# Kernel tuning notes

Measured on AMD Instinct MI355X. Metric: run time of the kernel, lower is better.

The kernel has to match this reference:

```python
import jax, jax.numpy as jnp
import numpy as np

U, I, D = 100000, 100000, 64
B, T = 16384, 1_638_400
R = 5  # rating levels 1..5


def setup_inputs() -> dict:
    key = jax.random.key(0)
    ks = jax.random.split(key, 8)
    return {
        "user_idx": jax.random.randint(ks[0], (B,), 0, U, dtype=jnp.int32),
        "item_idx": jax.random.randint(ks[1], (B,), 0, I, dtype=jnp.int32),
        "flat_items": jax.random.randint(ks[2], (T,), 0, I, dtype=jnp.int32),
        "seg_ids": jnp.sort(jax.random.randint(ks[3], (T,), 0, B * R, dtype=jnp.int32)),
        "user_emb": (jax.random.uniform(ks[4], (U, D), dtype=jnp.float32) - 0.5) * 0.01,
        "item_emb": (jax.random.uniform(ks[5], (I, D), dtype=jnp.float32) - 0.5) * 0.01,
        "Mr": (jax.random.uniform(ks[6], (I, D), dtype=jnp.float32) - 0.5) * 0.01,
        "user_bias": jnp.zeros((U,), dtype=jnp.float32),
        "item_bias": jnp.zeros((I,), dtype=jnp.float32),
        "global_avg": jnp.float32(3.5),
    }


def reference(user_idx, item_idx, flat_items, seg_ids, user_emb, item_emb, Mr, user_bias, item_bias, global_avg):
    num_seg = B * R  # segment = sample_i * 5 + (rating - 1)
    # Original torch code does Mr_ik(rate_dict).sum() -> scalar over ALL dims,
    # then broadcasts that scalar onto the latent_dim vector UuMpc[i].
    row_sum = Mr[flat_items].sum(axis=-1)  # [T] per-item full-row sum
    # Emulate `rate_dict.remove(item_idx[i])`: mask out the target item of this sample.
    match = flat_items == item_idx[seg_ids // R]  # [T]
    contrib = jnp.where(match, 0.0, row_sum)
    seg_sum = jax.ops.segment_sum(contrib, seg_ids, num_segments=num_seg)  # [B*5]
    cnt = jax.ops.segment_sum(jnp.where(match, 0.0, 1.0), seg_ids, num_segments=num_seg)
    per_seg = jnp.where(cnt > 0, seg_sum / jnp.sqrt(jnp.maximum(cnt, 1.0)), 0.0)
    uu_mpc = per_seg.reshape(B, R).sum(axis=-1)  # [B] scalar per sample
    user_vec = user_emb[user_idx] + uu_mpc[:, None]  # broadcast scalar over latent dim
    item_vec = item_emb[item_idx]
    rui = (user_vec * item_vec).sum(axis=-1) + user_bias[user_idx] + item_bias[item_idx] + global_avg
    return jnp.clip(rui, 1.0, 5.0)
```

## Files before the change

kernel.cpp:

```cpp
#include <hip/hip_runtime.h>

#define U_N 100000
#define I_N 100000
#define D_N 64
#define B_N 16384
#define T_N 1638400
#define R_N 5

#define RS_THREADS (I_N * 16)
#define BD_THREADS (T_N / 4)
#define K1_THREADS (RS_THREADS + BD_THREADS)

__global__ void prep_kernel(const float* __restrict__ Mr,
                            const int* __restrict__ seg_ids,
                            float* __restrict__ rowsum,
                            int* __restrict__ sample_start) {
    int gtid = blockIdx.x * blockDim.x + threadIdx.x;
    if (gtid < RS_THREADS) {
        int row = gtid >> 4;
        int sub = gtid & 15;
        const float4* p = (const float4*)(Mr + (long)row * D_N);
        float4 v4 = p[sub];
        float v = v4.x + v4.y + v4.z + v4.w;
        v += __shfl_xor(v, 1);
        v += __shfl_xor(v, 2);
        v += __shfl_xor(v, 4);
        v += __shfl_xor(v, 8);
        if (sub == 0) rowsum[row] = v;
    } else {
        int t4 = gtid - RS_THREADS;
        if (t4 >= BD_THREADS) return;
        int base = t4 * 4;
        int4 s4 = ((const int4*)seg_ids)[t4];
        int sv[5];
        sv[0] = (base == 0) ? -1 : seg_ids[base - 1];
        sv[1] = s4.x; sv[2] = s4.y; sv[3] = s4.z; sv[4] = s4.w;
        #pragma unroll
        for (int j = 0; j < 4; ++j) {
            int sp = sv[j], sc = sv[j + 1];
            if (sc > sp) {
                int b_lo = (sp + 5) / 5;
                int b_hi = sc / 5;
                for (int b = b_lo; b <= b_hi; ++b) sample_start[b] = base + j;
            }
        }
        if (base + 4 == T_N) {
            for (int b = sv[4] / 5 + 1; b <= B_N; ++b) sample_start[b] = T_N;
        }
    }
}

__global__ void sample_kernel(const int* __restrict__ user_idx,
                              const int* __restrict__ item_idx,
                              const int* __restrict__ flat_items,
                              const int* __restrict__ seg_ids,
                              const float* __restrict__ user_emb,
                              const float* __restrict__ item_emb,
                              const float* __restrict__ user_bias,
                              const float* __restrict__ item_bias,
                              const float* __restrict__ global_avg,
                              const float* __restrict__ rowsum,
                              const int* __restrict__ sample_start,
                              float* __restrict__ out) {
    __shared__ float s_sum[4][5];
    __shared__ int   s_cnt[4][5];

    int w    = threadIdx.x >> 6;
    int lane = threadIdx.x & 63;
    int b    = blockIdx.x * 4 + w;
    if (b >= B_N) return;

    if (lane < R_N) { s_sum[w][lane] = 0.f; s_cnt[w][lane] = 0; }
    __syncthreads();

    int lo = sample_start[b];
    int hi = sample_start[b + 1];
    int target = item_idx[b];

    for (int t = lo + lane; t < hi; t += 64) {
        int sg = seg_ids[t];
        int it = flat_items[t];
        if (it != target) {
            int r = sg - b * R_N;
            atomicAdd(&s_sum[w][r], rowsum[it]);
            atomicAdd(&s_cnt[w][r], 1);
        }
    }
    __syncthreads();

    float uu = 0.f;
    if (lane == 0) {
        #pragma unroll
        for (int r = 0; r < R_N; ++r) {
            int c = s_cnt[w][r];
            if (c > 0) uu += s_sum[w][r] / sqrtf((float)c);
        }
    }

    int u = user_idx[b];
    float ue = user_emb[(long)u * D_N + lane];
    float ie = item_emb[(long)target * D_N + lane];
    float dot = ue * ie;
    float isum = ie;
    #pragma unroll
    for (int off = 32; off >= 1; off >>= 1) {
        dot  += __shfl_xor(dot, off);
        isum += __shfl_xor(isum, off);
    }
    if (lane == 0) {
        float rui = dot + uu * isum + user_bias[u] + item_bias[target] + global_avg[0];
        rui = fminf(fmaxf(rui, 1.0f), 5.0f);
        out[b] = rui;
    }
}

extern "C" void kernel_launch(void* const* d_in, const int* in_sizes, int n_in,
                              void* d_out, int out_size, void* d_ws, size_t ws_size,
                              hipStream_t stream) {
    const int*   user_idx   = (const int*)d_in[0];
    const int*   item_idx   = (const int*)d_in[1];
    const int*   flat_items = (const int*)d_in[2];
    const int*   seg_ids    = (const int*)d_in[3];
    const float* user_emb   = (const float*)d_in[4];
    const float* item_emb   = (const float*)d_in[5];
    const float* Mr         = (const float*)d_in[6];
    const float* user_bias  = (const float*)d_in[7];
    const float* item_bias  = (const float*)d_in[8];
    const float* global_avg = (const float*)d_in[9];
    float* out = (float*)d_out;

    float* rowsum       = (float*)d_ws;
    int*   sample_start = (int*)(rowsum + I_N);

    prep_kernel<<<(K1_THREADS + 255) / 256, 256, 0, stream>>>(
        Mr, seg_ids, rowsum, sample_start);
    sample_kernel<<<B_N / 4, 256, 0, stream>>>(
        user_idx, item_idx, flat_items, seg_ids, user_emb, item_emb,
        user_bias, item_bias, global_avg, rowsum, sample_start, out);
}
```

Before: 147.3 us.

## Replace shared-memory atomics with register accumulators and wave shuffle reductions

Per-rating sums and counts are now kept in per-lane registers and reduced across the wavefront with shuffles, replacing the LDS atomics and both block-wide barriers. The segment loop is unrolled four ways so several seg_ids, flat_items and rowsum gathers are in flight at once, and the embedding loads are hoisted ahead of the loop to overlap their latency. In exchange, the final reduction now runs ten extra shuffle chains and each lane uses more registers.

```diff
diff --git a/kernel.cpp b/kernel.cpp
--- a/kernel.cpp
+++ b/kernel.cpp
@@ -62,52 +62,67 @@
                               const float* __restrict__ rowsum,
                               const int* __restrict__ sample_start,
                               float* __restrict__ out) {
-    __shared__ float s_sum[4][5];
-    __shared__ int   s_cnt[4][5];
-
-    int w    = threadIdx.x >> 6;
     int lane = threadIdx.x & 63;
-    int b    = blockIdx.x * 4 + w;
+    int b    = (blockIdx.x * blockDim.x + threadIdx.x) >> 6;
     if (b >= B_N) return;
 
-    if (lane < R_N) { s_sum[w][lane] = 0.f; s_cnt[w][lane] = 0; }
-    __syncthreads();
+    int u      = user_idx[b];
+    int target = item_idx[b];
+    float ue = user_emb[(long)u * D_N + lane];
+    float ie = item_emb[(long)target * D_N + lane];
 
     int lo = sample_start[b];
     int hi = sample_start[b + 1];
-    int target = item_idx[b];
+    int base5 = b * R_N;
 
-    for (int t = lo + lane; t < hi; t += 64) {
-        int sg = seg_ids[t];
-        int it = flat_items[t];
-        if (it != target) {
-            int r = sg - b * R_N;
-            atomicAdd(&s_sum[w][r], rowsum[it]);
-            atomicAdd(&s_cnt[w][r], 1);
+    float acc[R_N] = {0.f, 0.f, 0.f, 0.f, 0.f};
+    float cnt[R_N] = {0.f, 0.f, 0.f, 0.f, 0.f};
+
+    for (int t0 = lo + lane; t0 < hi; t0 += 256) {
+        int  sg[4], fi[4];
+        bool ok[4];
+        #pragma unroll
+        for (int k = 0; k < 4; ++k) {
+            int t = t0 + 64 * k;
+            ok[k] = (t < hi);
+            if (ok[k]) { sg[k] = seg_ids[t]; fi[k] = flat_items[t]; }
         }
-    }
-    __syncthreads();
-
-    float uu = 0.f;
-    if (lane == 0) {
+        float rv[4];
         #pragma unroll
-        for (int r = 0; r < R_N; ++r) {
-            int c = s_cnt[w][r];
-            if (c > 0) uu += s_sum[w][r] / sqrtf((float)c);
+        for (int k = 0; k < 4; ++k) {
+            if (ok[k]) rv[k] = rowsum[fi[k]];
+        }
+        #pragma unroll
+        for (int k = 0; k < 4; ++k) {
+            if (ok[k] && fi[k] != target) {
+                int r = sg[k] - base5;
+                #pragma unroll
+                for (int rr = 0; rr < R_N; ++rr) {
+                    if (r == rr) { acc[rr] += rv[k]; cnt[rr] += 1.f; }
+                }
+            }
         }
     }
 
-    int u = user_idx[b];
-    float ue = user_emb[(long)u * D_N + lane];
-    float ie = item_emb[(long)target * D_N + lane];
     float dot = ue * ie;
     float isum = ie;
     #pragma unroll
     for (int off = 32; off >= 1; off >>= 1) {
+        #pragma unroll
+        for (int rr = 0; rr < R_N; ++rr) {
+            acc[rr] += __shfl_xor(acc[rr], off);
+            cnt[rr] += __shfl_xor(cnt[rr], off);
+        }
         dot  += __shfl_xor(dot, off);
         isum += __shfl_xor(isum, off);
     }
+
     if (lane == 0) {
+        float uu = 0.f;
+        #pragma unroll
+        for (int rr = 0; rr < R_N; ++rr) {
+            if (cnt[rr] > 0.f) uu += acc[rr] / sqrtf(cnt[rr]);
+        }
         float rui = dot + uu * isum + user_bias[u] + item_bias[target] + global_avg[0];
         rui = fminf(fmaxf(rui, 1.0f), 5.0f);
         out[b] = rui;
```

After: 141.1 us. -4.2%, faster.

## Use per-segment offsets and ballot match counting instead of shared atomics

Applied to the files above, without the earlier changes.

The prep kernel now builds per-segment start offsets rather than per-sample offsets. The sample kernel derives each segment's count from those offsets minus a ballot/popcount tally of target-item matches. It then accumulates rowsum times a precomputed rsqrt weight in registers and reduces with shuffles, which removes the seg_ids reads, the LDS atomics and the __syncthreads. The cost is a second pass over flat_items whenever a sample has more than 128 entries, plus extra per-element branching to pick the segment weight.

```diff
diff --git a/kernel.cpp b/kernel.cpp
--- a/kernel.cpp
+++ b/kernel.cpp
@@ -6,6 +6,7 @@
 #define B_N 16384
 #define T_N 1638400
 #define R_N 5
+#define NSEG (B_N * R_N)
 
 #define RS_THREADS (I_N * 16)
 #define BD_THREADS (T_N / 4)
@@ -14,7 +15,7 @@
 __global__ void prep_kernel(const float* __restrict__ Mr,
                             const int* __restrict__ seg_ids,
                             float* __restrict__ rowsum,
-                            int* __restrict__ sample_start) {
+                            int* __restrict__ seg_start) {
     int gtid = blockIdx.x * blockDim.x + threadIdx.x;
     if (gtid < RS_THREADS) {
         int row = gtid >> 4;
@@ -32,20 +33,32 @@
         if (t4 >= BD_THREADS) return;
         int base = t4 * 4;
         int4 s4 = ((const int4*)seg_ids)[t4];
-        int sv[5];
-        sv[0] = (base == 0) ? -1 : seg_ids[base - 1];
-        sv[1] = s4.x; sv[2] = s4.y; sv[3] = s4.z; sv[4] = s4.w;
+        int sv0 = (base == 0) ? -1 : seg_ids[base - 1];
+        int sv1 = s4.x, sv2 = s4.y, sv3 = s4.z, sv4 = s4.w;
+        for (int s = sv0 + 1; s <= sv1; ++s) seg_start[s] = base + 0;
+        for (int s = sv1 + 1; s <= sv2; ++s) seg_start[s] = base + 1;
+        for (int s = sv2 + 1; s <= sv3; ++s) seg_start[s] = base + 2;
+        for (int s = sv3 + 1; s <= sv4; ++s) seg_start[s] = base + 3;
+        if (base + 4 == T_N) {
+            for (int s = sv4 + 1; s <= NSEG; ++s) seg_start[s] = T_N;
+        }
+    }
+}
+
+__device__ __forceinline__ void count_matches(unsigned long long m, int tb,
+                                              int e0, int e1, int e2, int e3,
+                                              int e4, int e5, int* mcnt) {
+    if (m) {
+        int ea[6] = {e0, e1, e2, e3, e4, e5};
         #pragma unroll
-        for (int j = 0; j < 4; ++j) {
-            int sp = sv[j], sc = sv[j + 1];
-            if (sc > sp) {
-                int b_lo = (sp + 5) / 5;
-                int b_hi = sc / 5;
-                for (int b = b_lo; b <= b_hi; ++b) sample_start[b] = base + j;
+        for (int r = 0; r < 5; ++r) {
+            int a = ea[r] - tb;     a = a < 0 ? 0 : (a > 64 ? 64 : a);
+            int bb = ea[r + 1] - tb; bb = bb < 0 ? 0 : (bb > 64 ? 64 : bb);
+            if (bb > a) {
+                unsigned long long hiM = (bb == 64) ? ~0ULL : ((1ULL << bb) - 1ULL);
+                unsigned long long loM = (1ULL << a) - 1ULL;
+                mcnt[r] += __popcll(m & hiM & ~loM);
             }
-        }
-        if (base + 4 == T_N) {
-            for (int b = sv[4] / 5 + 1; b <= B_N; ++b) sample_start[b] = T_N;
         }
     }
 }
@@ -53,62 +66,95 @@
 __global__ void sample_kernel(const int* __restrict__ user_idx,
                               const int* __restrict__ item_idx,
                               const int* __restrict__ flat_items,
-                              const int* __restrict__ seg_ids,
                               const float* __restrict__ user_emb,
                               const float* __restrict__ item_emb,
                               const float* __restrict__ user_bias,
                               const float* __restrict__ item_bias,
                               const float* __restrict__ global_avg,
                               const float* __restrict__ rowsum,
-                              const int* __restrict__ sample_start,
+                              const int* __restrict__ seg_start,
                               float* __restrict__ out) {
-    __shared__ float s_sum[4][5];
-    __shared__ int   s_cnt[4][5];
-
-    int w    = threadIdx.x >> 6;
     int lane = threadIdx.x & 63;
-    int b    = blockIdx.x * 4 + w;
+    int b    = (blockIdx.x * blockDim.x + threadIdx.x) >> 6;
     if (b >= B_N) return;
 
-    if (lane < R_N) { s_sum[w][lane] = 0.f; s_cnt[w][lane] = 0; }
-    __syncthreads();
+    int u      = user_idx[b];
+    int target = item_idx[b];
+    float ue = user_emb[(long)u * D_N + lane];
+    float ie = item_emb[(long)target * D_N + lane];
 
-    int lo = sample_start[b];
-    int hi = sample_start[b + 1];
-    int target = item_idx[b];
+    int e0 = seg_start[b * R_N + 0];
+    int e1 = seg_start[b * R_N + 1];
+    int e2 = seg_start[b * R_N + 2];
+    int e3 = seg_start[b * R_N + 3];
+    int e4 = seg_start[b * R_N + 4];
+    int e5 = seg_start[b * R_N + 5];
+    int lo = e0, hi = e5;
 
-    for (int t = lo + lane; t < hi; t += 64) {
-        int sg = seg_ids[t];
-        int it = flat_items[t];
-        if (it != target) {
-            int r = sg - b * R_N;
-            atomicAdd(&s_sum[w][r], rowsum[it]);
-            atomicAdd(&s_cnt[w][r], 1);
-        }
+    int t0 = lo + lane, t1 = lo + 64 + lane;
+    bool ok0 = t0 < hi, ok1 = t1 < hi;
+    int fi0 = -1, fi1 = -1;
+    float rv0 = 0.f, rv1 = 0.f;
+    if (ok0) fi0 = flat_items[t0];
+    if (ok1) fi1 = flat_items[t1];
+    if (ok0) rv0 = rowsum[fi0];
+    if (ok1) rv1 = rowsum[fi1];
+
+    int mcnt[5] = {0, 0, 0, 0, 0};
+    unsigned long long m0 = __ballot(ok0 && fi0 == target);
+    unsigned long long m1 = __ballot(ok1 && fi1 == target);
+    count_matches(m0, lo,      e0, e1, e2, e3, e4, e5, mcnt);
+    count_matches(m1, lo + 64, e0, e1, e2, e3, e4, e5, mcnt);
+    for (int tb = lo + 128; tb < hi; tb += 64) {
+        int t = tb + lane;
+        bool ok = t < hi;
+        int fi = ok ? flat_items[t] : -1;
+        unsigned long long m = __ballot(ok && fi == target);
+        count_matches(m, tb, e0, e1, e2, e3, e4, e5, mcnt);
     }
-    __syncthreads();
 
-    float uu = 0.f;
-    if (lane == 0) {
-        #pragma unroll
-        for (int r = 0; r < R_N; ++r) {
-            int c = s_cnt[w][r];
-            if (c > 0) uu += s_sum[w][r] / sqrtf((float)c);
+    int c0 = (e1 - e0) - mcnt[0];
+    int c1 = (e2 - e1) - mcnt[1];
+    int c2 = (e3 - e2) - mcnt[2];
+    int c3 = (e4 - e3) - mcnt[3];
+    int c4 = (e5 - e4) - mcnt[4];
+    float w0 = c0 > 0 ? rsqrtf((float)c0) : 0.f;
+    float w1 = c1 > 0 ? rsqrtf((float)c1) : 0.f;
+    float w2 = c2 > 0 ? rsqrtf((float)c2) : 0.f;
+    float w3 = c3 > 0 ? rsqrtf((float)c3) : 0.f;
+    float w4 = c4 > 0 ? rsqrtf((float)c4) : 0.f;
+
+    float acc = 0.f;
+    if (ok0 && fi0 != target) {
+        float w = t0 >= e1 ? (t0 >= e2 ? (t0 >= e3 ? (t0 >= e4 ? w4 : w3) : w2) : w1) : w0;
+        acc += rv0 * w;
+    }
+    if (ok1 && fi1 != target) {
+        float w = t1 >= e1 ? (t1 >= e2 ? (t1 >= e3 ? (t1 >= e4 ? w4 : w3) : w2) : w1) : w0;
+        acc += rv1 * w;
+    }
+    for (int tb = lo + 128; tb < hi; tb += 64) {
+        int t = tb + lane;
+        if (t < hi) {
+            int fi = flat_items[t];
+            if (fi != target) {
+                float rv = rowsum[fi];
+                float w = t >= e1 ? (t >= e2 ? (t >= e3 ? (t >= e4 ? w4 : w3) : w2) : w1) : w0;
+                acc += rv * w;
+            }
         }
     }
 
-    int u = user_idx[b];
-    float ue = user_emb[(long)u * D_N + lane];
-    float ie = item_emb[(long)target * D_N + lane];
     float dot = ue * ie;
     float isum = ie;
     #pragma unroll
     for (int off = 32; off >= 1; off >>= 1) {
+        acc  += __shfl_xor(acc, off);
         dot  += __shfl_xor(dot, off);
         isum += __shfl_xor(isum, off);
     }
     if (lane == 0) {
-        float rui = dot + uu * isum + user_bias[u] + item_bias[target] + global_avg[0];
+        float rui = dot + acc * isum + user_bias[u] + item_bias[target] + global_avg[0];
         rui = fminf(fmaxf(rui, 1.0f), 5.0f);
         out[b] = rui;
     }
@@ -129,12 +175,12 @@
     const float* global_avg = (const float*)d_in[9];
     float* out = (float*)d_out;
 
-    float* rowsum       = (float*)d_ws;
-    int*   sample_start = (int*)(rowsum + I_N);
+    float* rowsum    = (float*)d_ws;
+    int*   seg_start = (int*)(rowsum + I_N);
 
     prep_kernel<<<(K1_THREADS + 255) / 256, 256, 0, stream>>>(
-        Mr, seg_ids, rowsum, sample_start);
+        Mr, seg_ids, rowsum, seg_start);
     sample_kernel<<<B_N / 4, 256, 0, stream>>>(
-        user_idx, item_idx, flat_items, seg_ids, user_emb, item_emb,
-        user_bias, item_bias, global_avg, rowsum, sample_start, out);
+        user_idx, item_idx, flat_items, user_emb, item_emb,
+        user_bias, item_bias, global_avg, rowsum, seg_start, out);
 }
```

Result: faster. 136.8 us (median of 2 runs) (-7.1%).
